# Kernel optimization log

Hardware: AMD Instinct MI355X
Metric: run time of the kernel (lower is better)

## Reference

```python
import jax, jax.numpy as jnp
import numpy as np
from jax import lax

EPS = 1e-6  # LayerNorm2d eps


def _ln2d(x, w, b):
    # channel-wise LayerNorm over dim 1 of [B,C,H,W]
    mu = jnp.mean(x, axis=1, keepdims=True)
    var = jnp.mean((x - mu) ** 2, axis=1, keepdims=True)
    return (x - mu) / jnp.sqrt(var + EPS) * w[None, :, None, None] + b[None, :, None, None]


def _conv1x1(x, w, b):
    # w: [O, C]
    return jnp.einsum('bchw,oc->bohw', x, w) + b[None, :, None, None]


def _dconv(x, w, b):
    # 3x3 conv, dilation 4, padding 4 -> same H,W. w: [O, C, 3, 3]
    y = lax.conv_general_dilated(x, w, window_strides=(1, 1),
                                 padding=((4, 4), (4, 4)), rhs_dilation=(4, 4),
                                 dimension_numbers=('NCHW', 'OIHW', 'NCHW'))
    return y + b[None, :, None, None]


def _forward(x_l, x_r, nl_w, nl_b, nr_w, nr_b, lp1_w, lp1_b, rp1_w, rp1_b,
             dl_w, dl_b, dr_w, dr_b, lp2_w, lp2_b, rp2_w, rp2_b, beta, gamma):
    c = x_l.shape[1]
    scale = c ** (-0.5)
    N_l = _ln2d(x_l, nl_w, nl_b)
    N_r = _ln2d(x_r, nr_w, nr_b)
    V_l = jnp.transpose(_conv1x1(x_l, lp2_w, lp2_b), (0, 2, 3, 1))   # [B,H,W,C]
    V_r = jnp.transpose(_conv1x1(x_r, rp2_w, rp2_b), (0, 2, 3, 1))
    Q_l = jnp.transpose(_conv1x1(N_l, lp1_w, lp1_b), (0, 2, 3, 1))   # [B,H,W,C]
    Q_r = jnp.transpose(_conv1x1(N_r, rp1_w, rp1_b), (0, 2, 3, 1))
    K_l_T = jnp.transpose(_dconv(N_l, dl_w, dl_b), (0, 2, 1, 3))     # [B,H,C,W]
    K_r_T = jnp.transpose(_dconv(N_r, dr_w, dr_b), (0, 2, 1, 3))
    # per-row cross attention: [B,H,W,W]
    attn_r2l = jnp.einsum('bhwc,bhcv->bhwv', Q_l, K_r_T) * scale
    attn_l2r = jnp.einsum('bhwc,bhcv->bhwv', Q_r, K_l_T) * scale
    F_r2l = jnp.einsum('bhwv,bhvc->bhwc', jax.nn.softmax(attn_r2l, axis=-1), V_r)
    F_l2r = jnp.einsum('bhwv,bhvc->bhwc', jax.nn.softmax(attn_l2r, axis=-1), V_l)
    F_r2l = jnp.transpose(F_r2l, (0, 3, 1, 2)) * beta   # [B,C,H,W]
    F_l2r = jnp.transpose(F_l2r, (0, 3, 1, 2)) * gamma
    return x_l + F_r2l, x_r + F_l2r


def setup_inputs() -> dict:
    key = jax.random.key(0)
    ks = jax.random.split(key, 12)
    B, C, H, W = 2, 128, 192, 512
    s = 0.02
    rn = lambda k, shp: s * jax.random.normal(k, shp, jnp.float32)
    return {
        'x_l': jax.random.normal(ks[0], (B, C, H, W), jnp.float32),
        'x_r': jax.random.normal(ks[1], (B, C, H, W), jnp.float32),
        'nl_w': jnp.ones((C,), jnp.float32), 'nl_b': jnp.zeros((C,), jnp.float32),
        'nr_w': jnp.ones((C,), jnp.float32), 'nr_b': jnp.zeros((C,), jnp.float32),
        'lp1_w': rn(ks[2], (C, C)), 'lp1_b': jnp.zeros((C,), jnp.float32),
        'rp1_w': rn(ks[3], (C, C)), 'rp1_b': jnp.zeros((C,), jnp.float32),
        'dl_w': rn(ks[4], (C, C, 3, 3)), 'dl_b': jnp.zeros((C,), jnp.float32),
        'dr_w': rn(ks[5], (C, C, 3, 3)), 'dr_b': jnp.zeros((C,), jnp.float32),
        'lp2_w': rn(ks[6], (C, C)), 'lp2_b': jnp.zeros((C,), jnp.float32),
        'rp2_w': rn(ks[7], (C, C)), 'rp2_b': jnp.zeros((C,), jnp.float32),
        'beta': 0.1 * jax.random.normal(ks[8], (1, C, 1, 1), jnp.float32),
        'gamma': 0.1 * jax.random.normal(ks[9], (1, C, 1, 1), jnp.float32),
    }


def reference(x_l, x_r, nl_w, nl_b, nr_w, nr_b, lp1_w, lp1_b, rp1_w, rp1_b,
              dl_w, dl_b, dr_w, dr_b, lp2_w, lp2_b, rp2_w, rp2_b, beta, gamma):
    return _forward(x_l, x_r, nl_w, nl_b, nr_w, nr_b, lp1_w, lp1_b, rp1_w, rp1_b,
                    dl_w, dl_b, dr_w, dr_b, lp2_w, lp2_b, rp2_w, rp2_b, beta, gamma)
```

## Files before the change

kernel.cpp:

```cpp
#include <hip/hip_runtime.h>
#include <stdint.h>

#define CC 128
#define HH 192
#define WW 512
#define BB 2
#define HW (HH*WW)
#define CHW (CC*HW)
#define TENS (BB*CHW)

typedef __attribute__((ext_vector_type(8))) short bf16x8;
typedef __attribute__((ext_vector_type(4))) float f32x4;
typedef __attribute__((ext_vector_type(4))) unsigned short u16x4;

__device__ __forceinline__ unsigned short f2bf(float f) {
    union { float f; unsigned u; } v; v.f = f;
    return (unsigned short)((v.u + 0x7FFFu + ((v.u >> 16) & 1u)) >> 16);
}
__device__ __forceinline__ float bf2f(unsigned short u) {
    union { unsigned u; float f; } v; v.u = ((unsigned)u) << 16;
    return v.f;
}
__device__ __forceinline__ uint32_t cvtpk(float lo, float hi) {
    uint32_t r;
    asm("v_cvt_pk_bf16_f32 %0, %1, %2" : "=v"(r) : "v"(lo), "v"(hi));
    return r;
}
__device__ __forceinline__ f32x4 MFMA(bf16x8 a, bf16x8 b, f32x4 c) {
    return __builtin_amdgcn_mfma_f32_16x16x32_bf16(a, b, c, 0, 0, 0);
}

__global__ __launch_bounds__(256) void wcast_k(
    const float* __restrict__ dlw, const float* __restrict__ drw,
    unsigned short* __restrict__ wd)
{
    int i = blockIdx.x * 256 + threadIdx.x;
    if (i >= 2 * 9 * CC * CC) return;
    int side = i / (9 * CC * CC);
    int r = i % (9 * CC * CC);
    int tap = r / (CC * CC);
    int r2 = r % (CC * CC);
    int o = r2 >> 7, c = r2 & 127;
    const float* src = side ? drw : dlw;
    wd[i] = f2bf(src[((size_t)o * CC + c) * 9 + tap]);
}

__global__ __launch_bounds__(256) void lnv_k(
    const float* __restrict__ xl, const float* __restrict__ xr,
    const float* __restrict__ nlw, const float* __restrict__ nlb,
    const float* __restrict__ nrw, const float* __restrict__ nrb,
    const float* __restrict__ wlp, const float* __restrict__ blp,
    const float* __restrict__ wrp, const float* __restrict__ brp,
    unsigned short* __restrict__ ntl, unsigned short* __restrict__ ntr,
    unsigned short* __restrict__ vlo, unsigned short* __restrict__ vro)
{
    const int side = blockIdx.y;
    const float* x  = side ? xr : xl;
    const float* nw = side ? nrw : nlw;
    const float* nb = side ? nrb : nlb;
    const float* wv = side ? wrp : wlp;
    const float* bv = side ? brp : blp;
    unsigned short* nt = side ? ntr : ntl;
    unsigned short* vo = side ? vro : vlo;
    const int bid = blockIdx.x;
    const int wt = bid & 7, h = (bid >> 3) % HH, b = bid / (8 * HH);
    const int w0 = wt * 64;
    const int t = threadIdx.x;

    __shared__ unsigned short sA[64][136];
    __shared__ unsigned short sB[128][136];
    __shared__ float red[8][64];
    __shared__ float smu[64], srs[64];

    {
        const int w = t & 63, cg = t >> 6;
        const float* xp = x + (size_t)b * CHW + (size_t)h * WW + w0 + w;
        float s = 0.f, q = 0.f;
        for (int i = 0; i < 16; i++) {
            int c = cg * 32 + i * 2;
            float v0 = xp[(size_t)c * HW];
            float v1 = xp[(size_t)(c + 1) * HW];
            *(uint32_t*)&sA[w][c] = cvtpk(v0, v1);
            s += v0 + v1; q += v0 * v0 + v1 * v1;
        }
        red[cg][w] = s; red[4 + cg][w] = q;
    }
    for (int it = 0; it < 16; it++) {
        int f = it * 1024 + t * 4;
        int o = f >> 7, c = f & 127;
        float4 v = *(const float4*)(wv + o * CC + c);
        *(uint32_t*)&sB[o][c]     = cvtpk(v.x, v.y);
        *(uint32_t*)&sB[o][c + 2] = cvtpk(v.z, v.w);
    }
    __syncthreads();
    if (t < 64) {
        float S = red[0][t] + red[1][t] + red[2][t] + red[3][t];
        float Q = red[4][t] + red[5][t] + red[6][t] + red[7][t];
        float mu = S * (1.f / CC);
        float var = fmaxf(Q * (1.f / CC) - mu * mu, 0.f);
        smu[t] = mu; srs[t] = rsqrtf(var + 1e-6f);
    }
    __syncthreads();
    {
        const int w = t >> 2, c0 = (t & 3) * 32;
        const float mu = smu[w], rs = srs[w];
        unsigned short* np = nt + ((size_t)(b * HH + h) * WW + w0 + w) * CC;
        for (int i = 0; i < 32; i += 2) {
            int c = c0 + i;
            float v0 = (bf2f(sA[w][c]) - mu) * rs * nw[c] + nb[c];
            float v1 = (bf2f(sA[w][c + 1]) - mu) * rs * nw[c + 1] + nb[c + 1];
            *(uint32_t*)&np[c] = cvtpk(v0, v1);
        }
    }
    const int wid = t >> 6, l = t & 63, lr = l & 15, lg = l >> 4;
    f32x4 acc[8] = {};
    for (int kk = 0; kk < 4; kk++) {
        bf16x8 a = *(const bf16x8*)&sA[wid * 16 + lr][kk * 32 + lg * 8];
#pragma unroll
        for (int n_ = 0; n_ < 8; n_++) {
            bf16x8 bb = *(const bf16x8*)&sB[n_ * 16 + lr][kk * 32 + lg * 8];
            acc[n_] = MFMA(a, bb, acc[n_]);
        }
    }
    unsigned short* vp = vo + ((size_t)(b * HH + h) * CC) * WW + w0;
    for (int n_ = 0; n_ < 8; n_++) {
        int o = n_ * 16 + lr;
        float bias = bv[o];
        uint2 uu;
        uu.x = cvtpk(acc[n_][0] + bias, acc[n_][1] + bias);
        uu.y = cvtpk(acc[n_][2] + bias, acc[n_][3] + bias);
        *(uint2*)&vp[(size_t)o * WW + wid * 16 + lg * 4] = uu;
    }
}

__global__ __launch_bounds__(256) void dconv_k(
    const unsigned short* __restrict__ ntl, const unsigned short* __restrict__ ntr,
    const unsigned short* __restrict__ wd,
    const float* __restrict__ dlb, const float* __restrict__ drb,
    unsigned short* __restrict__ klo, unsigned short* __restrict__ kro)
{
    const int side = blockIdx.y;
    const unsigned short* nt = side ? ntr : ntl;
    const unsigned short* wdp = wd + (size_t)side * 9 * CC * CC;
    const float* bd = side ? drb : dlb;
    unsigned short* ko = side ? kro : klo;
    const int bid0 = blockIdx.x;
    const int lgc = (bid0 & 7) * 192 + (bid0 >> 3);
    const int wt = lgc & 3;
    const int hb = lgc >> 2;
    const int h = hb % HH, b = hb / HH;
    const int w0 = wt * 128;
    const int t = threadIdx.x;
    const int wid = t >> 6, l = t & 63, lr = l & 15, lg = l >> 4;
    const int whalf = wid & 1, ohalf = wid >> 1;

    __shared__ unsigned short sA[136][136];
    __shared__ unsigned short sB[128][136];

    f32x4 acc[4][4] = {};
    for (int dy = 0; dy < 3; dy++) {
        const int hh = h + 4 * (dy - 1);
        const bool hok = (hh >= 0 && hh < HH);
        __syncthreads();
        for (int f = t * 8; f < 136 * 128; f += 2048) {
            int wloc = f >> 7, c = f & 127;
            int w = w0 - 4 + wloc;
            bf16x8 v = {0, 0, 0, 0, 0, 0, 0, 0};
            if (hok && w >= 0 && w < WW)
                v = *(const bf16x8*)(nt + ((size_t)(b * HH + hh) * WW + w) * CC + c);
            *(bf16x8*)&sA[wloc][c] = v;
        }
        for (int dx = 0; dx < 3; dx++) {
            __syncthreads();
            const int tap = dy * 3 + dx;
            for (int it = 0; it < 8; it++) {
                int f = it * 2048 + t * 8;
                *(bf16x8*)&sB[f >> 7][f & 127] =
                    *(const bf16x8*)(wdp + (size_t)tap * CC * CC + f);
            }
            __syncthreads();
            for (int kk = 0; kk < 4; kk++) {
                bf16x8 af[4], bf_[4];
#pragma unroll
                for (int g = 0; g < 4; g++)
                    af[g] = *(const bf16x8*)&sA[whalf * 64 + g * 16 + lr + 4 * dx][kk * 32 + lg * 8];
#pragma unroll
                for (int n_ = 0; n_ < 4; n_++)
                    bf_[n_] = *(const bf16x8*)&sB[ohalf * 64 + n_ * 16 + lr][kk * 32 + lg * 8];
#pragma unroll
                for (int g = 0; g < 4; g++)
#pragma unroll
                    for (int n_ = 0; n_ < 4; n_++)
                        acc[g][n_] = MFMA(af[g], bf_[n_], acc[g][n_]);
            }
        }
    }
    unsigned short* kp = ko + ((size_t)(b * HH + h) * WW + w0) * CC;
    for (int g = 0; g < 4; g++)
        for (int n_ = 0; n_ < 4; n_++) {
            int o = ohalf * 64 + n_ * 16 + lr;
            float bias = bd[o];
            for (int j = 0; j < 4; j++) {
                int w = whalf * 64 + g * 16 + lg * 4 + j;
                kp[(size_t)w * CC + o] = f2bf(acc[g][n_][j] + bias);
            }
        }
}

__global__ __launch_bounds__(256, 2) void attn_k(
    const unsigned short* __restrict__ ntl, const unsigned short* __restrict__ ntr,
    const unsigned short* __restrict__ kl,  const unsigned short* __restrict__ kr,
    const unsigned short* __restrict__ vtl, const unsigned short* __restrict__ vtr,
    const float* __restrict__ lp1w, const float* __restrict__ lp1b,
    const float* __restrict__ rp1w, const float* __restrict__ rp1b,
    const float* __restrict__ xl, const float* __restrict__ xr,
    const float* __restrict__ beta, const float* __restrict__ gamma,
    float* __restrict__ out)
{
    __shared__ __align__(16) char smem[70656];
    unsigned short* sQ  = (unsigned short*)smem;
    unsigned short* sW  = (unsigned short*)(smem + 34816);
    unsigned short* sKt = (unsigned short*)(smem + 34816);
    unsigned short* sVt = (unsigned short*)(smem + 52224);

    const int dir = blockIdx.z;
    const unsigned short* nq  = dir ? ntr : ntl;
    const unsigned short* kws = dir ? kl : kr;
    const unsigned short* vws = dir ? vtl : vtr;
    const float* wq   = dir ? rp1w : lp1w;
    const float* bq   = dir ? rp1b : lp1b;
    const float* xres = dir ? xr : xl;
    const float* mult = dir ? gamma : beta;
    float* op = out + (size_t)dir * TENS;

    const int bid = blockIdx.x;
    const int xcd = bid & 7;
    const int s   = bid >> 3;
    const int qb  = s & 3;
    const int bh  = xcd + 8 * (s >> 2);
    const int q0  = qb * 128;
    const int t = threadIdx.x;
    const int wid = t >> 6, l = t & 63, lr = l & 15, lg = l >> 4;

    const unsigned short* ksrc = kws + (size_t)bh * WW * CC;
    const unsigned short* vsrc = vws + (size_t)bh * CC * WW;

    bf16x8 kreg[4], vreg[4];
#pragma unroll
    for (int it = 0; it < 4; it++) {
        int f = it * 2048 + t * 8;
        kreg[it] = *(const bf16x8*)(ksrc + f);
    }
#pragma unroll
    for (int it = 0; it < 4; it++) {
        int f = it * 2048 + t * 8;
        int c = f >> 6, k = f & 63;
        vreg[it] = *(const bf16x8*)(vsrc + (size_t)c * WW + k);
    }

    {
        const unsigned short* nsrc = nq + ((size_t)bh * WW + q0) * CC;
        for (int it = 0; it < 8; it++) {
            int f = it * 2048 + t * 8;
            *(bf16x8*)&sQ[(f >> 7) * 136 + (f & 127)] = *(const bf16x8*)(nsrc + f);
        }
        for (int it = 0; it < 16; it++) {
            int f = it * 1024 + t * 4;
            int o = f >> 7, c = f & 127;
            float4 v = *(const float4*)(wq + o * CC + c);
            *(uint32_t*)&sW[o * 136 + c]     = cvtpk(v.x, v.y);
            *(uint32_t*)&sW[o * 136 + c + 2] = cvtpk(v.z, v.w);
        }
    }
    __syncthreads();
    {
        f32x4 qacc[2][8] = {};
        for (int kk = 0; kk < 4; kk++) {
            bf16x8 a0 = *(const bf16x8*)&sQ[(wid * 32 + lr) * 136 + kk * 32 + lg * 8];
            bf16x8 a1 = *(const bf16x8*)&sQ[(wid * 32 + 16 + lr) * 136 + kk * 32 + lg * 8];
#pragma unroll
            for (int n_ = 0; n_ < 8; n_++) {
                bf16x8 b = *(const bf16x8*)&sW[(n_ * 16 + lr) * 136 + kk * 32 + lg * 8];
                qacc[0][n_] = MFMA(a0, b, qacc[0][n_]);
                qacc[1][n_] = MFMA(a1, b, qacc[1][n_]);
            }
        }
        const float SCL = 0.08838834764831845f * 1.4426950408889634f;
        __syncthreads();
#pragma unroll
        for (int mg = 0; mg < 2; mg++)
#pragma unroll
            for (int n_ = 0; n_ < 8; n_++) {
                float bias = bq[n_ * 16 + lr];
#pragma unroll
                for (int j = 0; j < 4; j++)
                    sQ[(wid * 32 + mg * 16 + lg * 4 + j) * 136 + n_ * 16 + lr] =
                        f2bf((qacc[mg][n_][j] + bias) * SCL);
            }
    }
    __syncthreads();
    bf16x8 qf[2][4];
#pragma unroll
    for (int qg = 0; qg < 2; qg++)
#pragma unroll
        for (int kk = 0; kk < 4; kk++)
            qf[qg][kk] = *(const bf16x8*)&sQ[(wid * 32 + qg * 16 + lr) * 136 + kk * 32 + lg * 8];

    f32x4 oacc[8][2] = {};
    float mrow[2] = {-1e30f, -1e30f};
    float lrow[2] = {0.f, 0.f};
    const int src0 = lr + ((l & 16) << 1);
    const int src1 = src0 + 16;
    const int hi = lg >> 1;

    for (int kb = 0; kb < 8; kb++) {
        __syncthreads();
#pragma unroll
        for (int it = 0; it < 4; it++) {
            int f = it * 2048 + t * 8;
            *(bf16x8*)&sKt[(f >> 7) * 136 + (f & 127)] = kreg[it];
        }
#pragma unroll
        for (int it = 0; it < 4; it++) {
            int f = it * 2048 + t * 8;
            int c = f >> 6, k = f & 63;
            *(bf16x8*)&sVt[c * 72 + k] = vreg[it];
        }
        if (kb < 7) {
#pragma unroll
            for (int it = 0; it < 4; it++) {
                int f = it * 2048 + t * 8;
                kreg[it] = *(const bf16x8*)(ksrc + (kb + 1) * 64 * CC + f);
            }
#pragma unroll
            for (int it = 0; it < 4; it++) {
                int f = it * 2048 + t * 8;
                int c = f >> 6, k = f & 63;
                vreg[it] = *(const bf16x8*)(vsrc + (size_t)c * WW + (kb + 1) * 64 + k);
            }
        }
        __syncthreads();
        f32x4 sacc[2][4] = {};
        __builtin_amdgcn_s_setprio(1);
        for (int kk = 0; kk < 4; kk++)
#pragma unroll
            for (int n_ = 0; n_ < 4; n_++) {
                bf16x8 kf = *(const bf16x8*)&sKt[(n_ * 16 + lr) * 136 + kk * 32 + lg * 8];
                sacc[0][n_] = MFMA(kf, qf[0][kk], sacc[0][n_]);
                sacc[1][n_] = MFMA(kf, qf[1][kk], sacc[1][n_]);
            }
        __builtin_amdgcn_s_setprio(0);
        float al[2];
#pragma unroll
        for (int qg = 0; qg < 2; qg++) {
            float pm = sacc[qg][0][0];
#pragma unroll
            for (int n_ = 0; n_ < 4; n_++)
#pragma unroll
                for (int j = 0; j < 4; j++) pm = fmaxf(pm, sacc[qg][n_][j]);
            pm = fmaxf(pm, __shfl_xor(pm, 16, 64));
            pm = fmaxf(pm, __shfl_xor(pm, 32, 64));
            float mn = fmaxf(mrow[qg], pm);
            al[qg] = exp2f(mrow[qg] - mn);
            mrow[qg] = mn;
            float rs = 0.f;
#pragma unroll
            for (int n_ = 0; n_ < 4; n_++)
#pragma unroll
                for (int j = 0; j < 4; j++) {
                    float e = exp2f(sacc[qg][n_][j] - mn);
                    sacc[qg][n_][j] = e;
                    rs += e;
                }
            rs += __shfl_xor(rs, 16, 64);
            rs += __shfl_xor(rs, 32, 64);
            lrow[qg] = lrow[qg] * al[qg] + rs;
        }
#pragma unroll
        for (int n_ = 0; n_ < 8; n_++)
#pragma unroll
            for (int qg = 0; qg < 2; qg++) {
                f32x4 o = oacc[n_][qg];
                o[0] *= al[qg]; o[1] *= al[qg]; o[2] *= al[qg]; o[3] *= al[qg];
                oacc[n_][qg] = o;
            }
        uint32_t pk[2][4][2];
#pragma unroll
        for (int qg = 0; qg < 2; qg++)
#pragma unroll
            for (int n_ = 0; n_ < 4; n_++) {
                pk[qg][n_][0] = cvtpk(sacc[qg][n_][0], sacc[qg][n_][1]);
                pk[qg][n_][1] = cvtpk(sacc[qg][n_][2], sacc[qg][n_][3]);
            }
#pragma unroll
        for (int kk = 0; kk < 2; kk++) {
            union { uint32_t u[4]; bf16x8 v; } pf[2];
#pragma unroll
            for (int qg = 0; qg < 2; qg++) {
                uint32_t q00 = __shfl(pk[qg][kk * 2][0],     src0, 64);
                uint32_t q01 = __shfl(pk[qg][kk * 2][1],     src0, 64);
                uint32_t q02 = __shfl(pk[qg][kk * 2][0],     src1, 64);
                uint32_t q03 = __shfl(pk[qg][kk * 2][1],     src1, 64);
                uint32_t q10 = __shfl(pk[qg][kk * 2 + 1][0], src0, 64);
                uint32_t q11 = __shfl(pk[qg][kk * 2 + 1][1], src0, 64);
                uint32_t q12 = __shfl(pk[qg][kk * 2 + 1][0], src1, 64);
                uint32_t q13 = __shfl(pk[qg][kk * 2 + 1][1], src1, 64);
                pf[qg].u[0] = hi ? q10 : q00;
                pf[qg].u[1] = hi ? q11 : q01;
                pf[qg].u[2] = hi ? q12 : q02;
                pf[qg].u[3] = hi ? q13 : q03;
            }
            __builtin_amdgcn_s_setprio(1);
#pragma unroll
            for (int n_ = 0; n_ < 8; n_++) {
                bf16x8 va = *(const bf16x8*)&sVt[(n_ * 16 + lr) * 72 + kk * 32 + lg * 8];
                oacc[n_][0] = MFMA(va, pf[0].v, oacc[n_][0]);
                oacc[n_][1] = MFMA(va, pf[1].v, oacc[n_][1]);
            }
            __builtin_amdgcn_s_setprio(0);
        }
    }

    const float inv0 = 1.f / lrow[0], inv1 = 1.f / lrow[1];
    const int b = bh / HH, h = bh % HH;
    const int w_0 = q0 + wid * 32 + lr;
    const float* xp0 = xres + (size_t)b * CHW + (size_t)h * WW + w_0;
    float* outp0 = op + (size_t)b * CHW + (size_t)h * WW + w_0;
#pragma unroll
    for (int n_ = 0; n_ < 8; n_++) {
        float4 m4 = *(const float4*)&mult[n_ * 16 + lg * 4];
#pragma unroll
        for (int j = 0; j < 4; j++) {
            int c = n_ * 16 + lg * 4 + j;
            float mj = (&m4.x)[j];
            outp0[(size_t)c * HW]      = xp0[(size_t)c * HW]      + oacc[n_][0][j] * inv0 * mj;
            outp0[(size_t)c * HW + 16] = xp0[(size_t)c * HW + 16] + oacc[n_][1][j] * inv1 * mj;
        }
    }
}

extern "C" void kernel_launch(void* const* d_in, const int* in_sizes, int n_in,
                              void* d_out, int out_size, void* d_ws, size_t ws_size,
                              hipStream_t stream)
{
    const float* xl   = (const float*)d_in[0];
    const float* xr   = (const float*)d_in[1];
    const float* nlw  = (const float*)d_in[2];
    const float* nlb  = (const float*)d_in[3];
    const float* nrw  = (const float*)d_in[4];
    const float* nrb  = (const float*)d_in[5];
    const float* lp1w = (const float*)d_in[6];
    const float* lp1b = (const float*)d_in[7];
    const float* rp1w = (const float*)d_in[8];
    const float* rp1b = (const float*)d_in[9];
    const float* dlw  = (const float*)d_in[10];
    const float* dlb  = (const float*)d_in[11];
    const float* drw  = (const float*)d_in[12];
    const float* drb  = (const float*)d_in[13];
    const float* lp2w = (const float*)d_in[14];
    const float* lp2b = (const float*)d_in[15];
    const float* rp2w = (const float*)d_in[16];
    const float* rp2b = (const float*)d_in[17];
    const float* beta = (const float*)d_in[18];
    const float* gamma= (const float*)d_in[19];
    float* out = (float*)d_out;

    unsigned short* ws = (unsigned short*)d_ws;
    const size_t A = (size_t)TENS;
    unsigned short* Ntl = ws;
    unsigned short* Ntr = ws + A;
    unsigned short* Kl  = ws + 2 * A;
    unsigned short* Kr  = ws + 3 * A;
    unsigned short* Vtl = ws + 4 * A;
    unsigned short* Vtr = ws + 5 * A;
    unsigned short* Wd  = ws + 6 * A;

    wcast_k<<<dim3(1152), 256, 0, stream>>>(dlw, drw, Wd);
    lnv_k<<<dim3(3072, 2), 256, 0, stream>>>(xl, xr, nlw, nlb, nrw, nrb,
        lp2w, lp2b, rp2w, rp2b, Ntl, Ntr, Vtl, Vtr);
    dconv_k<<<dim3(1536, 2), 256, 0, stream>>>(Ntl, Ntr, Wd, dlb, drb, Kl, Kr);
    attn_k<<<dim3(1536, 1, 2), 256, 0, stream>>>(Ntl, Ntr, Kl, Kr, Vtl, Vtr,
        lp1w, lp1b, rp1w, rp1b, xl, xr, beta, gamma, out);
}
```

Before: 547.6 us.

## Pre-swizzle dconv weights, shrink attention LDS, add lazy softmax rescale

The weight-cast kernel now writes dilated-conv weights already in MFMA fragment order. dconv_k therefore loads B fragments straight from global memory instead of staging them through a second shared buffer with extra barriers, and asks for 3 blocks per CU. attn_k computes the Q projection in two 64-column halves so its weight buffer can be smaller, and it overlays K/V tiles on the Q region. That cuts LDS from about 69KB to 51KB so three blocks fit per CU. The online softmax also skips rescaling the running max and accumulators unless the new max exceeds the old one by more than 8 (log2 domain). This trades extra global/L2 traffic and more register pressure for fewer barriers, higher occupancy and fewer exp2/multiply operations.

```diff
diff --git a/kernel.cpp b/kernel.cpp
--- a/kernel.cpp
+++ b/kernel.cpp
@@ -36,11 +36,16 @@
 {
     int i = blockIdx.x * 256 + threadIdx.x;
     if (i >= 2 * 9 * CC * CC) return;
-    int side = i / (9 * CC * CC);
-    int r = i % (9 * CC * CC);
-    int tap = r / (CC * CC);
-    int r2 = r % (CC * CC);
-    int o = r2 >> 7, c = r2 & 127;
+    int e  = i & 7;
+    int l  = (i >> 3) & 63;
+    int n_ = (i >> 9) & 3;
+    int kk = (i >> 11) & 3;
+    int oh = (i >> 13) & 1;
+    int rest = i >> 14;
+    int tap = rest % 9;
+    int side = rest / 9;
+    int o = oh * 64 + n_ * 16 + (l & 15);
+    int c = kk * 32 + (l >> 4) * 8 + e;
     const float* src = side ? drw : dlw;
     wd[i] = f2bf(src[((size_t)o * CC + c) * 9 + tap]);
 }
@@ -133,15 +138,15 @@
     }
 }
 
-__global__ __launch_bounds__(256) void dconv_k(
+__global__ __launch_bounds__(256, 3) void dconv_k(
     const unsigned short* __restrict__ ntl, const unsigned short* __restrict__ ntr,
-    const unsigned short* __restrict__ wd,
+    const unsigned short* __restrict__ wfr,
     const float* __restrict__ dlb, const float* __restrict__ drb,
     unsigned short* __restrict__ klo, unsigned short* __restrict__ kro)
 {
     const int side = blockIdx.y;
     const unsigned short* nt = side ? ntr : ntl;
-    const unsigned short* wdp = wd + (size_t)side * 9 * CC * CC;
+    const unsigned short* wbase = wfr + (size_t)side * 9 * 16384;
     const float* bd = side ? drb : dlb;
     unsigned short* ko = side ? kro : klo;
     const int bid0 = blockIdx.x;
@@ -155,7 +160,6 @@
     const int whalf = wid & 1, ohalf = wid >> 1;
 
     __shared__ unsigned short sA[136][136];
-    __shared__ unsigned short sB[128][136];
 
     f32x4 acc[4][4] = {};
     for (int dy = 0; dy < 3; dy++) {
@@ -170,28 +174,26 @@
                 v = *(const bf16x8*)(nt + ((size_t)(b * HH + hh) * WW + w) * CC + c);
             *(bf16x8*)&sA[wloc][c] = v;
         }
+        __syncthreads();
+#pragma unroll
         for (int dx = 0; dx < 3; dx++) {
-            __syncthreads();
-            const int tap = dy * 3 + dx;
-            for (int it = 0; it < 8; it++) {
-                int f = it * 2048 + t * 8;
-                *(bf16x8*)&sB[f >> 7][f & 127] =
-                    *(const bf16x8*)(wdp + (size_t)tap * CC * CC + f);
-            }
-            __syncthreads();
+            const unsigned short* wtap =
+                wbase + (size_t)(dy * 3 + dx) * 16384 + ohalf * 8192 + l * 8;
+#pragma unroll
             for (int kk = 0; kk < 4; kk++) {
-                bf16x8 af[4], bf_[4];
+                bf16x8 bfr[4];
+#pragma unroll
+                for (int n_ = 0; n_ < 4; n_++)
+                    bfr[n_] = *(const bf16x8*)(wtap + (kk * 4 + n_) * 512);
+                bf16x8 af[4];
 #pragma unroll
                 for (int g = 0; g < 4; g++)
                     af[g] = *(const bf16x8*)&sA[whalf * 64 + g * 16 + lr + 4 * dx][kk * 32 + lg * 8];
 #pragma unroll
-                for (int n_ = 0; n_ < 4; n_++)
-                    bf_[n_] = *(const bf16x8*)&sB[ohalf * 64 + n_ * 16 + lr][kk * 32 + lg * 8];
-#pragma unroll
                 for (int g = 0; g < 4; g++)
 #pragma unroll
                     for (int n_ = 0; n_ < 4; n_++)
-                        acc[g][n_] = MFMA(af[g], bf_[n_], acc[g][n_]);
+                        acc[g][n_] = MFMA(af[g], bfr[n_], acc[g][n_]);
             }
         }
     }
@@ -207,7 +209,7 @@
         }
 }
 
-__global__ __launch_bounds__(256, 2) void attn_k(
+__global__ __launch_bounds__(256, 3) void attn_k(
     const unsigned short* __restrict__ ntl, const unsigned short* __restrict__ ntr,
     const unsigned short* __restrict__ kl,  const unsigned short* __restrict__ kr,
     const unsigned short* __restrict__ vtl, const unsigned short* __restrict__ vtr,
@@ -217,11 +219,11 @@
     const float* __restrict__ beta, const float* __restrict__ gamma,
     float* __restrict__ out)
 {
-    __shared__ __align__(16) char smem[70656];
+    __shared__ __align__(16) char smem[52224];
     unsigned short* sQ  = (unsigned short*)smem;
-    unsigned short* sW  = (unsigned short*)(smem + 34816);
-    unsigned short* sKt = (unsigned short*)(smem + 34816);
-    unsigned short* sVt = (unsigned short*)(smem + 52224);
+    unsigned short* sWh = (unsigned short*)(smem + 34816);
+    unsigned short* sKt = (unsigned short*)smem;
+    unsigned short* sVt = (unsigned short*)(smem + 17408);
 
     const int dir = blockIdx.z;
     const unsigned short* nq  = dir ? ntr : ntl;
@@ -264,29 +266,48 @@
             int f = it * 2048 + t * 8;
             *(bf16x8*)&sQ[(f >> 7) * 136 + (f & 127)] = *(const bf16x8*)(nsrc + f);
         }
-        for (int it = 0; it < 16; it++) {
+        for (int it = 0; it < 8; it++) {
             int f = it * 1024 + t * 4;
             int o = f >> 7, c = f & 127;
             float4 v = *(const float4*)(wq + o * CC + c);
-            *(uint32_t*)&sW[o * 136 + c]     = cvtpk(v.x, v.y);
-            *(uint32_t*)&sW[o * 136 + c + 2] = cvtpk(v.z, v.w);
+            *(uint32_t*)&sWh[o * 136 + c]     = cvtpk(v.x, v.y);
+            *(uint32_t*)&sWh[o * 136 + c + 2] = cvtpk(v.z, v.w);
+        }
+    }
+    f32x4 qacc[2][8] = {};
+    __syncthreads();
+    for (int kk = 0; kk < 4; kk++) {
+        bf16x8 a0 = *(const bf16x8*)&sQ[(wid * 32 + lr) * 136 + kk * 32 + lg * 8];
+        bf16x8 a1 = *(const bf16x8*)&sQ[(wid * 32 + 16 + lr) * 136 + kk * 32 + lg * 8];
+#pragma unroll
+        for (int n_ = 0; n_ < 4; n_++) {
+            bf16x8 b = *(const bf16x8*)&sWh[(n_ * 16 + lr) * 136 + kk * 32 + lg * 8];
+            qacc[0][n_] = MFMA(a0, b, qacc[0][n_]);
+            qacc[1][n_] = MFMA(a1, b, qacc[1][n_]);
+        }
+    }
+    __syncthreads();
+    for (int it = 0; it < 8; it++) {
+        int f = it * 1024 + t * 4;
+        int o = f >> 7, c = f & 127;
+        float4 v = *(const float4*)(wq + (o + 64) * CC + c);
+        *(uint32_t*)&sWh[o * 136 + c]     = cvtpk(v.x, v.y);
+        *(uint32_t*)&sWh[o * 136 + c + 2] = cvtpk(v.z, v.w);
+    }
+    __syncthreads();
+    for (int kk = 0; kk < 4; kk++) {
+        bf16x8 a0 = *(const bf16x8*)&sQ[(wid * 32 + lr) * 136 + kk * 32 + lg * 8];
+        bf16x8 a1 = *(const bf16x8*)&sQ[(wid * 32 + 16 + lr) * 136 + kk * 32 + lg * 8];
+#pragma unroll
+        for (int n_ = 0; n_ < 4; n_++) {
+            bf16x8 b = *(const bf16x8*)&sWh[(n_ * 16 + lr) * 136 + kk * 32 + lg * 8];
+            qacc[0][4 + n_] = MFMA(a0, b, qacc[0][4 + n_]);
+            qacc[1][4 + n_] = MFMA(a1, b, qacc[1][4 + n_]);
         }
     }
     __syncthreads();
     {
-        f32x4 qacc[2][8] = {};
-        for (int kk = 0; kk < 4; kk++) {
-            bf16x8 a0 = *(const bf16x8*)&sQ[(wid * 32 + lr) * 136 + kk * 32 + lg * 8];
-            bf16x8 a1 = *(const bf16x8*)&sQ[(wid * 32 + 16 + lr) * 136 + kk * 32 + lg * 8];
-#pragma unroll
-            for (int n_ = 0; n_ < 8; n_++) {
-                bf16x8 b = *(const bf16x8*)&sW[(n_ * 16 + lr) * 136 + kk * 32 + lg * 8];
-                qacc[0][n_] = MFMA(a0, b, qacc[0][n_]);
-                qacc[1][n_] = MFMA(a1, b, qacc[1][n_]);
-            }
-        }
         const float SCL = 0.08838834764831845f * 1.4426950408889634f;
-        __syncthreads();
 #pragma unroll
         for (int mg = 0; mg < 2; mg++)
 #pragma unroll
@@ -350,40 +371,52 @@
                 sacc[1][n_] = MFMA(kf, qf[1][kk], sacc[1][n_]);
             }
         __builtin_amdgcn_s_setprio(0);
-        float al[2];
+        float pm[2];
 #pragma unroll
         for (int qg = 0; qg < 2; qg++) {
-            float pm = sacc[qg][0][0];
+            float m_ = sacc[qg][0][0];
 #pragma unroll
             for (int n_ = 0; n_ < 4; n_++)
 #pragma unroll
-                for (int j = 0; j < 4; j++) pm = fmaxf(pm, sacc[qg][n_][j]);
-            pm = fmaxf(pm, __shfl_xor(pm, 16, 64));
-            pm = fmaxf(pm, __shfl_xor(pm, 32, 64));
-            float mn = fmaxf(mrow[qg], pm);
-            al[qg] = exp2f(mrow[qg] - mn);
-            mrow[qg] = mn;
+                for (int j = 0; j < 4; j++) m_ = fmaxf(m_, sacc[qg][n_][j]);
+            m_ = fmaxf(m_, __shfl_xor(m_, 16, 64));
+            m_ = fmaxf(m_, __shfl_xor(m_, 32, 64));
+            pm[qg] = m_;
+        }
+        bool need = (pm[0] - mrow[0] > 8.f) || (pm[1] - mrow[1] > 8.f);
+        if (__any(need)) {
+            float al[2];
+#pragma unroll
+            for (int qg = 0; qg < 2; qg++) {
+                float mn = fmaxf(mrow[qg], pm[qg]);
+                al[qg] = exp2f(mrow[qg] - mn);
+                mrow[qg] = mn;
+                lrow[qg] *= al[qg];
+            }
+#pragma unroll
+            for (int n_ = 0; n_ < 8; n_++)
+#pragma unroll
+                for (int qg = 0; qg < 2; qg++) {
+                    f32x4 o = oacc[n_][qg];
+                    o[0] *= al[qg]; o[1] *= al[qg]; o[2] *= al[qg]; o[3] *= al[qg];
+                    oacc[n_][qg] = o;
+                }
+        }
+#pragma unroll
+        for (int qg = 0; qg < 2; qg++) {
             float rs = 0.f;
 #pragma unroll
             for (int n_ = 0; n_ < 4; n_++)
 #pragma unroll
                 for (int j = 0; j < 4; j++) {
-                    float e = exp2f(sacc[qg][n_][j] - mn);
+                    float e = exp2f(sacc[qg][n_][j] - mrow[qg]);
                     sacc[qg][n_][j] = e;
                     rs += e;
                 }
             rs += __shfl_xor(rs, 16, 64);
             rs += __shfl_xor(rs, 32, 64);
-            lrow[qg] = lrow[qg] * al[qg] + rs;
-        }
-#pragma unroll
-        for (int n_ = 0; n_ < 8; n_++)
-#pragma unroll
-            for (int qg = 0; qg < 2; qg++) {
-                f32x4 o = oacc[n_][qg];
-                o[0] *= al[qg]; o[1] *= al[qg]; o[2] *= al[qg]; o[3] *= al[qg];
-                oacc[n_][qg] = o;
-            }
+            lrow[qg] += rs;
+        }
         uint32_t pk[2][4][2];
 #pragma unroll
         for (int qg = 0; qg < 2; qg++)
```

New measurement: 708.2 us. 29.3% more time.
